# Optimization experiments

Measured on AMD Instinct MI355X. Metric: run time of the kernel, lower is better.

The kernel has to match this reference:

```python
import jax, jax.numpy as jnp
import numpy as np

N, E = 10000, 320000
NF, HF = 256, 256  # input_nf/output_nf, hidden_nf
EPS = 1e-8


def setup_inputs() -> dict:
    key = jax.random.key(0)
    ks = jax.random.split(key, 20)
    h = jax.random.normal(ks[0], (N, NF), jnp.float32)
    coord = jax.random.normal(ks[1], (N, 3), jnp.float32)
    edge_index = jax.random.randint(ks[2], (2, E), 0, N, jnp.int32)

    def dense(k, fan_in, fan_out, scale=None):
        s = scale if scale is not None else 1.0 / np.sqrt(fan_in)
        W = jax.random.normal(k, (fan_in, fan_out), jnp.float32) * s
        b = jnp.zeros((fan_out,), jnp.float32)
        return W, b

    We1, be1 = dense(ks[3], 2 * NF + 1, HF)   # edge_mlp layer 1
    We2, be2 = dense(ks[4], HF, HF)           # edge_mlp layer 2
    Wn1, bn1 = dense(ks[5], HF + NF, HF)      # node_mlp layer 1
    Wn2, bn2 = dense(ks[6], HF, NF)           # node_mlp layer 2
    Wc1, bc1 = dense(ks[7], HF, HF)           # coord_mlp layer 1
    Wc2, bc2 = dense(ks[8], HF, 1, scale=0.001)  # coord_mlp final, tiny init (xavier gain=0.001)
    return dict(h=h, coord=coord, edge_index=edge_index,
                We1=We1, be1=be1, We2=We2, be2=be2,
                Wn1=Wn1, bn1=bn1, Wn2=Wn2, bn2=bn2,
                Wc1=Wc1, bc1=bc1, Wc2=Wc2, bc2=bc2)


def _segment_sum(data, seg_ids, num_segments):
    return jax.ops.segment_sum(data, seg_ids, num_segments=num_segments)


def reference(h, coord, edge_index, We1, be1, We2, be2, Wn1, bn1, Wn2, bn2, Wc1, bc1, Wc2, bc2):
    row, col = edge_index[0], edge_index[1]

    # coord2radial
    coord_diff = coord[row] - coord[col]                    # [E, 3]
    radial = jnp.sum(coord_diff ** 2, axis=1, keepdims=True)  # [E, 1]

    # edge model: MLP on [h_i, h_j, ||x_i - x_j||^2]
    edge_in = jnp.concatenate([h[row], h[col], radial], axis=1)  # [E, 2*NF+1]
    e = jax.nn.silu(edge_in @ We1 + be1)
    edge_feat = jax.nn.silu(e @ We2 + be2)                  # [E, HF]

    # coord model: coord_diff * coord_mlp(edge_feat), mean-aggregated
    c = jax.nn.silu(edge_feat @ Wc1 + bc1)
    trans = coord_diff * (c @ Wc2 + bc2)                    # [E, 3]
    agg_c = _segment_sum(trans, row, coord.shape[0])
    count = _segment_sum(jnp.ones_like(trans), row, coord.shape[0])
    coord_out = coord + agg_c / jnp.clip(count, 1.0)

    # node model: sum-aggregate edge features, concat with h, MLP
    agg_h = _segment_sum(edge_feat, row, h.shape[0])        # [N, HF]
    node_in = jnp.concatenate([h, agg_h], axis=1)           # [N, HF+NF]
    n = jax.nn.silu(node_in @ Wn1 + bn1)
    h_out = n @ Wn2 + bn2                                   # [N, NF]

    return h_out, coord_out
```

## Files before the change

kernel.cpp:

```cpp
#include <hip/hip_runtime.h>
#include <hip/hip_bf16.h>

typedef __bf16 bf16;
typedef __attribute__((ext_vector_type(8))) __bf16 bf16x8;
typedef __attribute__((ext_vector_type(4))) float f32x4;

static_assert(sizeof(bf16x8) == 16, "bf16x8 must be 16B");

constexpr int N_NODES = 10000;
constexpr int N_EDGES = 320000;
constexpr int KPAD    = 264;

__device__ __forceinline__ float rcp_f(float x) {
  float r; asm("v_rcp_f32 %0, %1" : "=v"(r) : "v"(x)); return r;
}
__device__ __forceinline__ float silu_f(float x) { return x * rcp_f(1.0f + __expf(-x)); }

__device__ __forceinline__ unsigned pk_bf16(float lo, float hi) {
  unsigned r;
  asm("v_cvt_pk_bf16_f32 %0, %1, %2" : "=v"(r) : "v"(lo), "v"(hi));
  return r;
}

__device__ __forceinline__ void mfmaT_k256(const bf16* __restrict__ WT, int wstride, int koff,
                                           const bf16* Albs, int w, int r, int q, f32x4 acc[4][4]) {
  for (int k0 = 0; k0 < 256; k0 += 32) {
    bf16x8 a[4], b[4];
#pragma unroll
    for (int mi = 0; mi < 4; ++mi)
      a[mi] = *(const bf16x8*)(WT + (size_t)(w * 64 + 16 * mi + r) * wstride + koff + k0 + q * 8);
#pragma unroll
    for (int ni = 0; ni < 4; ++ni)
      b[ni] = *(const bf16x8*)(Albs + (16 * ni + r) * KPAD + k0 + q * 8);
#pragma unroll
    for (int mi = 0; mi < 4; ++mi)
#pragma unroll
      for (int ni = 0; ni < 4; ++ni)
        acc[mi][ni] = __builtin_amdgcn_mfma_f32_16x16x32_bf16(a[mi], b[ni], acc[mi][ni], 0, 0, 0);
  }
}

__device__ __forceinline__ void mfmaT_k256_b1(const bf16* __restrict__ WT, int wstride, int koff,
                                              const bf16* Albs, int w, int r, int q, f32x4 acc[4]) {
  for (int k0 = 0; k0 < 256; k0 += 32) {
    bf16x8 a[4], b;
    b = *(const bf16x8*)(Albs + r * KPAD + k0 + q * 8);
#pragma unroll
    for (int mi = 0; mi < 4; ++mi)
      a[mi] = *(const bf16x8*)(WT + (size_t)(w * 64 + 16 * mi + r) * wstride + koff + k0 + q * 8);
#pragma unroll
    for (int mi = 0; mi < 4; ++mi)
      acc[mi] = __builtin_amdgcn_mfma_f32_16x16x32_bf16(a[mi], b, acc[mi], 0, 0, 0);
  }
}

__device__ __forceinline__ void transpose512(const float* __restrict__ W, bf16* __restrict__ WT,
                                             int local, int tid) {
  int tg = local * 256 + tid;
  int j = tg >> 6, k0 = (tg & 63) * 8;
  bf16x8 v;
#pragma unroll
  for (int i = 0; i < 8; ++i) v[i] = (bf16)W[(size_t)(k0 + i) * 256 + j];
  *(bf16x8*)(WT + (size_t)j * 512 + k0) = v;
}
__device__ __forceinline__ void transpose256(const float* __restrict__ W, bf16* __restrict__ WT,
                                             int local, int tid) {
  int tg = local * 256 + tid;
  int j = tg >> 5, k0 = (tg & 31) * 8;
  bf16x8 v;
#pragma unroll
  for (int i = 0; i < 8; ++i) v[i] = (bf16)W[(size_t)(k0 + i) * 256 + j];
  *(bf16x8*)(WT + (size_t)j * 256 + k0) = v;
}

__global__ __launch_bounds__(256) void prep_kernel(
    const float* __restrict__ h, const float* __restrict__ We1, const float* __restrict__ We2,
    const float* __restrict__ Wn1, const float* __restrict__ Wn2, const float* __restrict__ Wc1,
    const int* __restrict__ eidx,
    bf16* __restrict__ Hb, bf16* __restrict__ We1T, bf16* __restrict__ Wn1T,
    bf16* __restrict__ We2T, bf16* __restrict__ Wn2T, bf16* __restrict__ Wc1T,
    int* __restrict__ hist, float4* __restrict__ zero_base) {
  int bid = blockIdx.x, tid = threadIdx.x;
  if (bid < 1250) {
    int g = (bid * 256 + tid) * 8;
    float4 u = *(const float4*)(h + g);
    float4 v = *(const float4*)(h + g + 4);
    uint4 o;
    o.x = pk_bf16(u.x, u.y); o.y = pk_bf16(u.z, u.w);
    o.z = pk_bf16(v.x, v.y); o.w = pk_bf16(v.z, v.w);
    *(uint4*)(Hb + g) = o;
    return;
  }
  if (bid < 1474) {
    int wb = bid - 1250;
    if (wb < 64)       transpose512(We1, We1T, wb, tid);
    else if (wb < 128) transpose512(Wn1, Wn1T, wb - 64, tid);
    else if (wb < 160) transpose256(We2, We2T, wb - 128, tid);
    else if (wb < 192) transpose256(Wn2, Wn2T, wb - 160, tid);
    else               transpose256(Wc1, Wc1T, wb - 192, tid);
    return;
  }
  if (bid < 1787) {
    int t4 = (bid - 1474) * 256 + tid;
    if (t4 < 80000) {
      int4 e4 = *(const int4*)(eidx + t4 * 4);
      atomicAdd(&hist[e4.x], 1); atomicAdd(&hist[e4.y], 1);
      atomicAdd(&hist[e4.z], 1); atomicAdd(&hist[e4.w], 1);
    }
    return;
  }
  int zb = bid - 1787;
#pragma unroll
  for (int i = 0; i < 4; ++i) {
    int idx = zb * 1024 + i * 256 + tid;
    if (idx < 647500) zero_base[idx] = (float4){0.f, 0.f, 0.f, 0.f};
  }
}

__global__ __launch_bounds__(1024) void scan_kernel(const int* __restrict__ hist,
                                                    int* __restrict__ cursor) {
  __shared__ int sh[10000];
  __shared__ int partial[1024];
  int t = threadIdx.x;
  for (int i = 0; i < 10; ++i) { int idx = i * 1024 + t; if (idx < N_NODES) sh[idx] = hist[idx]; }
  __syncthreads();
  int s = 0;
  for (int i = 0; i < 10; ++i) { int idx = t * 10 + i; if (idx < N_NODES) s += sh[idx]; }
  partial[t] = s;
  __syncthreads();
  for (int d = 1; d < 1024; d <<= 1) {
    int v = (t >= d) ? partial[t - d] : 0;
    __syncthreads();
    partial[t] += v;
    __syncthreads();
  }
  int run = partial[t] - s;
  for (int i = 0; i < 10; ++i) {
    int idx = t * 10 + i;
    if (idx < N_NODES) { int hv = sh[idx]; sh[idx] = run; run += hv; }
  }
  __syncthreads();
  for (int i = 0; i < 10; ++i) {
    int idx = i * 1024 + t;
    if (idx < N_NODES) cursor[idx] = sh[idx];
  }
}

__global__ __launch_bounds__(256, 4) void scatter_gemm(
    const int* __restrict__ eidx, int* __restrict__ cursor, int2* __restrict__ rc,
    const bf16* __restrict__ Hb, const bf16* __restrict__ We1T,
    const float* __restrict__ be1, bf16* __restrict__ P, bf16* __restrict__ Q) {
  int bid = blockIdx.x, tid = threadIdx.x;
  if (bid < 313) {
    int t4 = bid * 256 + tid;
    if (t4 < 80000) {
      int e = t4 * 4;
      int4 r4 = *(const int4*)(eidx + e);
      int4 c4 = *(const int4*)(eidx + N_EDGES + e);
      int p0 = atomicAdd(&cursor[r4.x], 1); rc[p0] = (int2){r4.x, c4.x};
      int p1 = atomicAdd(&cursor[r4.y], 1); rc[p1] = (int2){r4.y, c4.y};
      int p2 = atomicAdd(&cursor[r4.z], 1); rc[p2] = (int2){r4.z, c4.z};
      int p3 = atomicAdd(&cursor[r4.w], 1); rc[p3] = (int2){r4.w, c4.w};
    }
    return;
  }
  int g = bid - 313;
  int w = tid >> 6, lane = tid & 63, r = lane & 15, q = lane >> 4;
  int m0 = (g >> 1) * 16;
  int koff = (g & 1) ? 256 : 0;
  bf16* OUT = (g & 1) ? Q : P;
  bool addb = !(g & 1);
  f32x4 acc[4];
#pragma unroll
  for (int mi = 0; mi < 4; ++mi) acc[mi] = (f32x4){0.f, 0.f, 0.f, 0.f};
  int m = m0 + r;

  for (int k0 = 0; k0 < 256; k0 += 32) {
    bf16x8 a[4], b;
    b = *(const bf16x8*)(Hb + (size_t)m * 256 + k0 + q * 8);
#pragma unroll
    for (int mi = 0; mi < 4; ++mi)
      a[mi] = *(const bf16x8*)(We1T + (size_t)(w * 64 + 16 * mi + r) * 512 + koff + k0 + q * 8);
#pragma unroll
    for (int mi = 0; mi < 4; ++mi)
      acc[mi] = __builtin_amdgcn_mfma_f32_16x16x32_bf16(a[mi], b, acc[mi], 0, 0, 0);
  }
#pragma unroll
  for (int mi = 0; mi < 4; ++mi) {
    int ch = w * 64 + 16 * mi + 4 * q;
    float4 bv = addb ? *(const float4*)(be1 + ch) : (float4){0.f, 0.f, 0.f, 0.f};
    uint2 o;
    o.x = pk_bf16(acc[mi][0] + bv.x, acc[mi][1] + bv.y);
    o.y = pk_bf16(acc[mi][2] + bv.z, acc[mi][3] + bv.w);
    *(uint2*)(OUT + (size_t)m * 256 + ch) = o;
  }
}

__global__ __launch_bounds__(256, 4) void edge_kernel(
    const float* __restrict__ coord, const int2* __restrict__ rc,
    const float* __restrict__ We1,
    const float* __restrict__ be2, const float* __restrict__ bc1,
    const float* __restrict__ Wc2, const float* __restrict__ bc2,
    const bf16* __restrict__ P, const bf16* __restrict__ Q,
    const bf16* __restrict__ We2T, const bf16* __restrict__ Wc1T,
    float* __restrict__ agg_h, float* __restrict__ agg_c) {
  __shared__ __align__(16) bf16 buf[64 * KPAD];
  __shared__ int s_row[64];
  __shared__ float s_rad[64], s_cd[64][3], s_part[64][4], s_scal[64];
  __shared__ int s_rs[65];
  __shared__ int s_nrun;

  int tid = threadIdx.x;
  int e0 = blockIdx.x * 64;
  int w = tid >> 6, lane = tid & 63, r = lane & 15, q = lane >> 4;

  int offv = (tid & 31) * 8;
  int esub = tid >> 5;
  int2 rc0 = rc[e0 + esub];
  bf16x8 pv = *(const bf16x8*)(P + (size_t)rc0.x * 256 + offv);
  bf16x8 qv = *(const bf16x8*)(Q + (size_t)rc0.y * 256 + offv);
  int2 rcn = rc[e0 + 8 + esub];
  float4 wa = *(const float4*)(We1 + 512 * 256 + offv);
  float4 wb = *(const float4*)(We1 + 512 * 256 + offv + 4);

  if (tid < 64) {
    int2 v = rc[e0 + tid];
    int ri = v.x, ci = v.y;
    s_row[tid] = ri;
    float dx = coord[3 * ri + 0] - coord[3 * ci + 0];
    float dy = coord[3 * ri + 1] - coord[3 * ci + 1];
    float dz = coord[3 * ri + 2] - coord[3 * ci + 2];
    s_cd[tid][0] = dx; s_cd[tid][1] = dy; s_cd[tid][2] = dz;
    s_rad[tid] = dx * dx + dy * dy + dz * dz;
  }
  __syncthreads();

  if (tid < 64) {
    bool bnd = (tid == 0) || (s_row[tid] != s_row[tid - 1]);
    unsigned long long m = __ballot(bnd);
    int rank = __popcll(m & ((1ull << tid) - 1ull));
    if (bnd) s_rs[rank] = tid;
    if (tid == 0) { int R = __popcll(m); s_nrun = R; s_rs[R] = 64; }
  }

#pragma unroll
  for (int p = 0; p < 8; ++p) {
    bf16x8 pvc = pv, qvc = qv;
    if (p < 7) {
      pv = *(const bf16x8*)(P + (size_t)rcn.x * 256 + offv);
      qv = *(const bf16x8*)(Q + (size_t)rcn.y * 256 + offv);
    }
    if (p < 6) rcn = rc[e0 + (p + 2) * 8 + esub];
    int e = p * 8 + esub;
    float rad = s_rad[e];
    float f0 = silu_f((float)pvc[0] + (float)qvc[0] + rad * wa.x);
    float f1 = silu_f((float)pvc[1] + (float)qvc[1] + rad * wa.y);
    float f2 = silu_f((float)pvc[2] + (float)qvc[2] + rad * wa.z);
    float f3 = silu_f((float)pvc[3] + (float)qvc[3] + rad * wa.w);
    float f4 = silu_f((float)pvc[4] + (float)qvc[4] + rad * wb.x);
    float f5 = silu_f((float)pvc[5] + (float)qvc[5] + rad * wb.y);
    float f6 = silu_f((float)pvc[6] + (float)qvc[6] + rad * wb.z);
    float f7 = silu_f((float)pvc[7] + (float)qvc[7] + rad * wb.w);
    uint4 o;
    o.x = pk_bf16(f0, f1); o.y = pk_bf16(f2, f3);
    o.z = pk_bf16(f4, f5); o.w = pk_bf16(f6, f7);
    *(uint4*)(buf + e * KPAD + offv) = o;
  }
  __syncthreads();

  {
    f32x4 acc[4][4];
#pragma unroll
    for (int mi = 0; mi < 4; ++mi)
#pragma unroll
      for (int ni = 0; ni < 4; ++ni) acc[mi][ni] = (f32x4){0.f, 0.f, 0.f, 0.f};
    mfmaT_k256(We2T, 256, 0, buf, w, r, q, acc);
    __syncthreads();
#pragma unroll
    for (int mi = 0; mi < 4; ++mi) {
      int ch = w * 64 + 16 * mi + 4 * q;
      float4 bv = *(const float4*)(be2 + ch);
#pragma unroll
      for (int ni = 0; ni < 4; ++ni) {
        int edge = 16 * ni + r;
        float f0 = silu_f(acc[mi][ni][0] + bv.x);
        float f1 = silu_f(acc[mi][ni][1] + bv.y);
        float f2 = silu_f(acc[mi][ni][2] + bv.z);
        float f3 = silu_f(acc[mi][ni][3] + bv.w);
        uint2 o; o.x = pk_bf16(f0, f1); o.y = pk_bf16(f2, f3);
        *(uint2*)(buf + edge * KPAD + ch) = o;
      }
    }
  }
  __syncthreads();

  f32x4 acc2[4][4];
#pragma unroll
  for (int mi = 0; mi < 4; ++mi)
#pragma unroll
    for (int ni = 0; ni < 4; ++ni) acc2[mi][ni] = (f32x4){0.f, 0.f, 0.f, 0.f};
  mfmaT_k256(Wc1T, 256, 0, buf, w, r, q, acc2);

  {
    int R = s_nrun;
    for (int rr = 0; rr < R; ++rr) {
      int st = s_rs[rr], en = s_rs[rr + 1];
      float s = 0.f;
      for (int e = st; e < en; ++e) s += (float)buf[e * KPAD + tid];
      atomicAdd(&agg_h[(size_t)s_row[st] * 256 + tid], s);
    }
  }

  {
    float p[4] = {0.f, 0.f, 0.f, 0.f};
#pragma unroll
    for (int mi = 0; mi < 4; ++mi) {
      int ch = w * 64 + 16 * mi + 4 * q;
      float4 bv = *(const float4*)(bc1 + ch);
      float4 wv = *(const float4*)(Wc2 + ch);
#pragma unroll
      for (int ni = 0; ni < 4; ++ni) {
        p[ni] += silu_f(acc2[mi][ni][0] + bv.x) * wv.x
               + silu_f(acc2[mi][ni][1] + bv.y) * wv.y
               + silu_f(acc2[mi][ni][2] + bv.z) * wv.z
               + silu_f(acc2[mi][ni][3] + bv.w) * wv.w;
      }
    }
#pragma unroll
    for (int ni = 0; ni < 4; ++ni) {
      float v = p[ni];
      v += __shfl_xor(v, 16, 64);
      v += __shfl_xor(v, 32, 64);
      if (q == 0) s_part[16 * ni + r][w] = v;
    }
  }
  __syncthreads();

  if (tid < 64)
    s_scal[tid] = s_part[tid][0] + s_part[tid][1] + s_part[tid][2] + s_part[tid][3] + bc2[0];
  __syncthreads();

  if (tid < 3) {
    int R = s_nrun;
    for (int rr = 0; rr < R; ++rr) {
      int st = s_rs[rr], en = s_rs[rr + 1];
      float s = 0.f;
      for (int e = st; e < en; ++e) s += s_cd[e][tid] * s_scal[e];
      atomicAdd(&agg_c[3 * s_row[st] + tid], s);
    }
  }
}

__global__ __launch_bounds__(256, 2) void node_kernel(
    const bf16* __restrict__ Hb, const float* __restrict__ agg_h,
    const int* __restrict__ hist, const float* __restrict__ coord, const float* __restrict__ agg_c,
    const bf16* __restrict__ Wn1T, const bf16* __restrict__ Wn2T,
    const float* __restrict__ bn1, const float* __restrict__ bn2,
    float* __restrict__ h_out, float* __restrict__ coord_out) {
  __shared__ __align__(16) bf16 buf[16 * KPAD];
  int tid = threadIdx.x, w = tid >> 6, lane = tid & 63, r = lane & 15, q = lane >> 4;
  int m0 = blockIdx.x * 16;
  int m = m0 + r;

  if (tid < 16) {
    int mm = m0 + tid;
    float c = (float)hist[mm]; if (c < 1.f) c = 1.f;
    coord_out[3 * mm + 0] = coord[3 * mm + 0] + agg_c[3 * mm + 0] / c;
    coord_out[3 * mm + 1] = coord[3 * mm + 1] + agg_c[3 * mm + 1] / c;
    coord_out[3 * mm + 2] = coord[3 * mm + 2] + agg_c[3 * mm + 2] / c;
  }

  f32x4 acc[4];
#pragma unroll
  for (int mi = 0; mi < 4; ++mi) acc[mi] = (f32x4){0.f, 0.f, 0.f, 0.f};
  for (int k0 = 0; k0 < 256; k0 += 32) {
    bf16x8 a[4], b;
    b = *(const bf16x8*)(Hb + (size_t)m * 256 + k0 + q * 8);
#pragma unroll
    for (int mi = 0; mi < 4; ++mi)
      a[mi] = *(const bf16x8*)(Wn1T + (size_t)(w * 64 + 16 * mi + r) * 512 + k0 + q * 8);
#pragma unroll
    for (int mi = 0; mi < 4; ++mi)
      acc[mi] = __builtin_amdgcn_mfma_f32_16x16x32_bf16(a[mi], b, acc[mi], 0, 0, 0);
  }
  for (int k0 = 0; k0 < 256; k0 += 32) {
    bf16x8 a[4], b;
    {
      const float* ap = agg_h + (size_t)m * 256 + k0 + q * 8;
      float4 u = *(const float4*)ap;
      float4 v = *(const float4*)(ap + 4);
      uint4 o;
      o.x = pk_bf16(u.x, u.y); o.y = pk_bf16(u.z, u.w);
      o.z = pk_bf16(v.x, v.y); o.w = pk_bf16(v.z, v.w);
      b = *(const bf16x8*)&o;
    }
#pragma unroll
    for (int mi = 0; mi < 4; ++mi)
      a[mi] = *(const bf16x8*)(Wn1T + (size_t)(w * 64 + 16 * mi + r) * 512 + 256 + k0 + q * 8);
#pragma unroll
    for (int mi = 0; mi < 4; ++mi)
      acc[mi] = __builtin_amdgcn_mfma_f32_16x16x32_bf16(a[mi], b, acc[mi], 0, 0, 0);
  }
  __syncthreads();
#pragma unroll
  for (int mi = 0; mi < 4; ++mi) {
    int ch = w * 64 + 16 * mi + 4 * q;
    float4 bv = *(const float4*)(bn1 + ch);
    float f0 = silu_f(acc[mi][0] + bv.x);
    float f1 = silu_f(acc[mi][1] + bv.y);
    float f2 = silu_f(acc[mi][2] + bv.z);
    float f3 = silu_f(acc[mi][3] + bv.w);
    uint2 o; o.x = pk_bf16(f0, f1); o.y = pk_bf16(f2, f3);
    *(uint2*)(buf + r * KPAD + ch) = o;
  }
  __syncthreads();
  f32x4 acc2[4];
#pragma unroll
  for (int mi = 0; mi < 4; ++mi) acc2[mi] = (f32x4){0.f, 0.f, 0.f, 0.f};
  mfmaT_k256_b1(Wn2T, 256, 0, buf, w, r, q, acc2);
#pragma unroll
  for (int mi = 0; mi < 4; ++mi) {
    int ch = w * 64 + 16 * mi + 4 * q;
    float4 bv = *(const float4*)(bn2 + ch);
    float4 o;
    o.x = acc2[mi][0] + bv.x;
    o.y = acc2[mi][1] + bv.y;
    o.z = acc2[mi][2] + bv.z;
    o.w = acc2[mi][3] + bv.w;
    *(float4*)(h_out + (size_t)m * 256 + ch) = o;
  }
}

extern "C" void kernel_launch(void* const* d_in, const int* in_sizes, int n_in,
                              void* d_out, int out_size, void* d_ws, size_t ws_size,
                              hipStream_t stream) {
  const float* h     = (const float*)d_in[0];
  const float* coord = (const float*)d_in[1];
  const int*   eidx  = (const int*)d_in[2];
  const float* We1 = (const float*)d_in[3];
  const float* be1 = (const float*)d_in[4];
  const float* We2 = (const float*)d_in[5];
  const float* be2 = (const float*)d_in[6];
  const float* Wn1 = (const float*)d_in[7];
  const float* bn1 = (const float*)d_in[8];
  const float* Wn2 = (const float*)d_in[9];
  const float* bn2 = (const float*)d_in[10];
  const float* Wc1 = (const float*)d_in[11];
  const float* bc1 = (const float*)d_in[12];
  const float* Wc2 = (const float*)d_in[13];
  const float* bc2 = (const float*)d_in[14];

  char* ws = (char*)d_ws;
  float* agg_h = (float*)(ws + 0);
  float* agg_c = (float*)(ws + 10240000);
  int*   hist  = (int*)  (ws + 10360000);
  int*   cursor= (int*)  (ws + 10440000);
  int2*  rc    = (int2*) (ws + 10480000);
  bf16* Hb   = (bf16*)(ws + 13040000);
  bf16* P    = (bf16*)(ws + 18160000);
  bf16* Q    = (bf16*)(ws + 23280000);
  bf16* We1T = (bf16*)(ws + 28400000);
  bf16* Wn1T = (bf16*)(ws + 28662144);
  bf16* We2T = (bf16*)(ws + 28924288);
  bf16* Wn2T = (bf16*)(ws + 29055360);
  bf16* Wc1T = (bf16*)(ws + 29186432);

  float* h_out = (float*)d_out;
  float* coord_out = h_out + (size_t)N_NODES * 256;

  hipMemsetAsync(hist, 0, 40000, stream);
  prep_kernel<<<2420, 256, 0, stream>>>(h, We1, We2, Wn1, Wn2, Wc1, eidx,
                                        Hb, We1T, Wn1T, We2T, Wn2T, Wc1T, hist,
                                        (float4*)agg_h);
  scan_kernel<<<1, 1024, 0, stream>>>(hist, cursor);
  scatter_gemm<<<1563, 256, 0, stream>>>(eidx, cursor, rc, Hb, We1T, be1, P, Q);
  edge_kernel<<<5000, 256, 0, stream>>>(coord, rc, We1, be2, bc1, Wc2, bc2,
                                        P, Q, We2T, Wc1T, agg_h, agg_c);
  node_kernel<<<625, 256, 0, stream>>>(Hb, agg_h, hist, coord, agg_c,
                                       Wn1T, Wn2T, bn1, bn2, h_out, coord_out);
}
```

Before: 405.2 us.

## Process 128 edges per edge-kernel block with 512 threads

```diff
diff --git a/kernel.cpp b/kernel.cpp
--- a/kernel.cpp
+++ b/kernel.cpp
@@ -22,16 +22,17 @@
   return r;
 }
 
-__device__ __forceinline__ void mfmaT_k256(const bf16* __restrict__ WT, int wstride, int koff,
-                                           const bf16* Albs, int w, int r, int q, f32x4 acc[4][4]) {
+__device__ __forceinline__ void mfmaT_k256e(const bf16* __restrict__ WT, int wstride,
+                                            const bf16* Albs, int eoff, int wch, int r, int q,
+                                            f32x4 acc[4][4]) {
   for (int k0 = 0; k0 < 256; k0 += 32) {
     bf16x8 a[4], b[4];
 #pragma unroll
     for (int mi = 0; mi < 4; ++mi)
-      a[mi] = *(const bf16x8*)(WT + (size_t)(w * 64 + 16 * mi + r) * wstride + koff + k0 + q * 8);
+      a[mi] = *(const bf16x8*)(WT + (size_t)(wch * 64 + 16 * mi + r) * wstride + k0 + q * 8);
 #pragma unroll
     for (int ni = 0; ni < 4; ++ni)
-      b[ni] = *(const bf16x8*)(Albs + (16 * ni + r) * KPAD + k0 + q * 8);
+      b[ni] = *(const bf16x8*)(Albs + (eoff + 16 * ni + r) * KPAD + k0 + q * 8);
 #pragma unroll
     for (int mi = 0; mi < 4; ++mi)
 #pragma unroll
@@ -196,7 +197,7 @@
   }
 }
 
-__global__ __launch_bounds__(256, 4) void edge_kernel(
+__global__ __launch_bounds__(512, 4) void edge_kernel(
     const float* __restrict__ coord, const int2* __restrict__ rc,
     const float* __restrict__ We1,
     const float* __restrict__ be2, const float* __restrict__ bc1,
@@ -204,26 +205,29 @@
     const bf16* __restrict__ P, const bf16* __restrict__ Q,
     const bf16* __restrict__ We2T, const bf16* __restrict__ Wc1T,
     float* __restrict__ agg_h, float* __restrict__ agg_c) {
-  __shared__ __align__(16) bf16 buf[64 * KPAD];
-  __shared__ int s_row[64];
-  __shared__ float s_rad[64], s_cd[64][3], s_part[64][4], s_scal[64];
-  __shared__ int s_rs[65];
+  __shared__ __align__(16) bf16 buf[128 * KPAD];
+  __shared__ int s_row[128];
+  __shared__ float s_rad[128], s_cd[128][3], s_part[128][4], s_scal[128];
+  __shared__ int s_rs[129];
   __shared__ int s_nrun;
+  __shared__ unsigned long long s_m[2];
 
   int tid = threadIdx.x;
-  int e0 = blockIdx.x * 64;
+  int e0 = blockIdx.x * 128;
   int w = tid >> 6, lane = tid & 63, r = lane & 15, q = lane >> 4;
+  int wch = w & 3, weh = w >> 2;
+  int eoff = weh * 64;
 
   int offv = (tid & 31) * 8;
   int esub = tid >> 5;
   int2 rc0 = rc[e0 + esub];
   bf16x8 pv = *(const bf16x8*)(P + (size_t)rc0.x * 256 + offv);
   bf16x8 qv = *(const bf16x8*)(Q + (size_t)rc0.y * 256 + offv);
-  int2 rcn = rc[e0 + 8 + esub];
+  int2 rcn = rc[e0 + 16 + esub];
   float4 wa = *(const float4*)(We1 + 512 * 256 + offv);
   float4 wb = *(const float4*)(We1 + 512 * 256 + offv + 4);
 
-  if (tid < 64) {
+  if (tid < 128) {
     int2 v = rc[e0 + tid];
     int ri = v.x, ci = v.y;
     s_row[tid] = ri;
@@ -235,12 +239,10 @@
   }
   __syncthreads();
 
-  if (tid < 64) {
+  if (tid < 128) {
     bool bnd = (tid == 0) || (s_row[tid] != s_row[tid - 1]);
     unsigned long long m = __ballot(bnd);
-    int rank = __popcll(m & ((1ull << tid) - 1ull));
-    if (bnd) s_rs[rank] = tid;
-    if (tid == 0) { int R = __popcll(m); s_nrun = R; s_rs[R] = 64; }
+    if ((tid & 63) == 0) s_m[tid >> 6] = m;
   }
 
 #pragma unroll
@@ -250,8 +252,8 @@
       pv = *(const bf16x8*)(P + (size_t)rcn.x * 256 + offv);
       qv = *(const bf16x8*)(Q + (size_t)rcn.y * 256 + offv);
     }
-    if (p < 6) rcn = rc[e0 + (p + 2) * 8 + esub];
-    int e = p * 8 + esub;
+    if (p < 6) rcn = rc[e0 + (p + 2) * 16 + esub];
+    int e = p * 16 + esub;
     float rad = s_rad[e];
     float f0 = silu_f((float)pvc[0] + (float)qvc[0] + rad * wa.x);
     float f1 = silu_f((float)pvc[1] + (float)qvc[1] + rad * wa.y);
@@ -268,21 +270,31 @@
   }
   __syncthreads();
 
+  if (tid < 128) {
+    unsigned long long m0 = s_m[0], m1 = s_m[1];
+    int c0 = __popcll(m0);
+    bool bnd = (tid == 0) || (s_row[tid] != s_row[tid - 1]);
+    unsigned long long mym = (tid < 64) ? m0 : m1;
+    int rank = __popcll(mym & ((1ull << (tid & 63)) - 1ull)) + (tid >= 64 ? c0 : 0);
+    if (bnd) s_rs[rank] = tid;
+    if (tid == 0) { int R = c0 + __popcll(m1); s_nrun = R; s_rs[R] = 128; }
+  }
+
   {
     f32x4 acc[4][4];
 #pragma unroll
     for (int mi = 0; mi < 4; ++mi)
 #pragma unroll
       for (int ni = 0; ni < 4; ++ni) acc[mi][ni] = (f32x4){0.f, 0.f, 0.f, 0.f};
-    mfmaT_k256(We2T, 256, 0, buf, w, r, q, acc);
+    mfmaT_k256e(We2T, 256, buf, eoff, wch, r, q, acc);
     __syncthreads();
 #pragma unroll
     for (int mi = 0; mi < 4; ++mi) {
-      int ch = w * 64 + 16 * mi + 4 * q;
+      int ch = wch * 64 + 16 * mi + 4 * q;
       float4 bv = *(const float4*)(be2 + ch);
 #pragma unroll
       for (int ni = 0; ni < 4; ++ni) {
-        int edge = 16 * ni + r;
+        int edge = eoff + 16 * ni + r;
         float f0 = silu_f(acc[mi][ni][0] + bv.x);
         float f1 = silu_f(acc[mi][ni][1] + bv.y);
         float f2 = silu_f(acc[mi][ni][2] + bv.z);
@@ -299,15 +311,21 @@
   for (int mi = 0; mi < 4; ++mi)
 #pragma unroll
     for (int ni = 0; ni < 4; ++ni) acc2[mi][ni] = (f32x4){0.f, 0.f, 0.f, 0.f};
-  mfmaT_k256(Wc1T, 256, 0, buf, w, r, q, acc2);
+  mfmaT_k256e(Wc1T, 256, buf, eoff, wch, r, q, acc2);
 
   {
     int R = s_nrun;
+    int g = tid >> 8, ch = tid & 255;
+    int base = g * 64, top = base + 64;
     for (int rr = 0; rr < R; ++rr) {
       int st = s_rs[rr], en = s_rs[rr + 1];
-      float s = 0.f;
-      for (int e = st; e < en; ++e) s += (float)buf[e * KPAD + tid];
-      atomicAdd(&agg_h[(size_t)s_row[st] * 256 + tid], s);
+      int lo = st > base ? st : base;
+      int hi = en < top ? en : top;
+      if (lo < hi) {
+        float s = 0.f;
+        for (int e = lo; e < hi; ++e) s += (float)buf[e * KPAD + ch];
+        atomicAdd(&agg_h[(size_t)s_row[lo] * 256 + ch], s);
+      }
     }
   }
 
@@ -315,7 +333,7 @@
     float p[4] = {0.f, 0.f, 0.f, 0.f};
 #pragma unroll
     for (int mi = 0; mi < 4; ++mi) {
-      int ch = w * 64 + 16 * mi + 4 * q;
+      int ch = wch * 64 + 16 * mi + 4 * q;
       float4 bv = *(const float4*)(bc1 + ch);
       float4 wv = *(const float4*)(Wc2 + ch);
 #pragma unroll
@@ -331,22 +349,28 @@
       float v = p[ni];
       v += __shfl_xor(v, 16, 64);
       v += __shfl_xor(v, 32, 64);
-      if (q == 0) s_part[16 * ni + r][w] = v;
-    }
-  }
-  __syncthreads();
-
-  if (tid < 64)
+      if (q == 0) s_part[eoff + 16 * ni + r][wch] = v;
+    }
+  }
+  __syncthreads();
+
+  if (tid < 128)
     s_scal[tid] = s_part[tid][0] + s_part[tid][1] + s_part[tid][2] + s_part[tid][3] + bc2[0];
   __syncthreads();
 
-  if (tid < 3) {
+  if (tid < 6) {
+    int comp = tid % 3, g = tid / 3;
+    int base = g * 64, top = base + 64;
     int R = s_nrun;
     for (int rr = 0; rr < R; ++rr) {
       int st = s_rs[rr], en = s_rs[rr + 1];
-      float s = 0.f;
-      for (int e = st; e < en; ++e) s += s_cd[e][tid] * s_scal[e];
-      atomicAdd(&agg_c[3 * s_row[st] + tid], s);
+      int lo = st > base ? st : base;
+      int hi = en < top ? en : top;
+      if (lo < hi) {
+        float s = 0.f;
+        for (int e = lo; e < hi; ++e) s += s_cd[e][comp] * s_scal[e];
+        atomicAdd(&agg_c[3 * s_row[lo] + comp], s);
+      }
     }
   }
 }
@@ -474,7 +498,7 @@
                                         (float4*)agg_h);
   scan_kernel<<<1, 1024, 0, stream>>>(hist, cursor);
   scatter_gemm<<<1563, 256, 0, stream>>>(eidx, cursor, rc, Hb, We1T, be1, P, Q);
-  edge_kernel<<<5000, 256, 0, stream>>>(coord, rc, We1, be2, bc1, Wc2, bc2,
+  edge_kernel<<<2500, 512, 0, stream>>>(coord, rc, We1, be2, bc1, Wc2, bc2,
                                         P, Q, We2T, Wc1T, agg_h, agg_c);
   node_kernel<<<625, 256, 0, stream>>>(Hb, agg_h, hist, coord, agg_c,
                                        Wn1T, Wn2T, bn1, bn2, h_out, coord_out);
```

After: 426.4 us. +5.2%, slower.
